# Performance work log

Measured on AMD Instinct MI355X. Metric: run time of the kernel, lower is better.

## Reference

```python
import jax, jax.numpy as jnp
import numpy as np

HOP = 2
N = 16384
HIDDEN = 64


def setup_inputs() -> dict:
    key = jax.random.key(0)
    k1, k2, k3 = jax.random.split(key, 3)
    user_embs = jax.random.normal(k1, (N, HIDDEN), dtype=jnp.float32)
    adj = jax.random.uniform(k2, (N, N), dtype=jnp.float32)
    # xavier-uniform-like scale for [2*HIDDEN, HIDDEN] weights
    limit = float(np.sqrt(6.0 / (2 * HIDDEN + HIDDEN)))
    W = jax.random.uniform(k3, (HOP, 2 * HIDDEN, HIDDEN), dtype=jnp.float32,
                           minval=-limit, maxval=limit)
    return {"user_embs": user_embs, "adj": adj, "W": W}


def reference(user_embs, adj, W):
    # DiffNet social GCN: hop rounds of aggregate -> concat -> dense -> tanh.
    # Dropout omitted (eval mode, training=False).
    x = user_embs
    for k in range(HOP):
        agg = adj @ x                                  # [N, H] neighbor aggregation
        x = jnp.tanh(jnp.concatenate([agg, x], axis=1) @ W[k])  # [N, H]
    return x
```

## Files before the change

kernel.cpp:

```cpp
#include <hip/hip_runtime.h>
#include <hip/hip_bf16.h>
#include <math.h>

#define NROWS 16384
#define HID 64
#define KSPLIT 8
#define KCH (NROWS / KSPLIT)

typedef __attribute__((ext_vector_type(8))) __bf16 bf16x8;
typedef __attribute__((ext_vector_type(4))) float f32x4;

__device__ inline f32x4 mfma16(bf16x8 a, bf16x8 b, f32x4 c) {
    return __builtin_amdgcn_mfma_f32_16x16x32_bf16(a, b, c, 0, 0, 0);
}

__device__ inline void split8v(const f32x4 v0, const f32x4 v1, bf16x8& h, bf16x8& l) {
    float f[8] = {v0[0], v0[1], v0[2], v0[3], v1[0], v1[1], v1[2], v1[3]};
#pragma unroll
    for (int j = 0; j < 8; ++j) {
        __bf16 hh = (__bf16)f[j];
        h[j] = hh;
        l[j] = (__bf16)(f[j] - (float)hh);
    }
}

__global__ __launch_bounds__(256) void pack_b(const float* __restrict__ x,
                                              __bf16* __restrict__ hi,
                                              __bf16* __restrict__ lo) {
    __shared__ float tile[32 * 64];
    const int kb = blockIdx.x;
    const f32x4* src = (const f32x4*)(x + (size_t)kb * 32 * 64);
    f32x4* dst = (f32x4*)tile;
    dst[threadIdx.x] = src[threadIdx.x];
    dst[threadIdx.x + 256] = src[threadIdx.x + 256];
    __syncthreads();
    const int t = threadIdx.x >> 6;
    const int l = threadIdx.x & 63;
    const int col = (t << 4) + (l & 15);
    const int krow = (l >> 4) * 8;
    bf16x8 h8, l8;
#pragma unroll
    for (int j = 0; j < 8; ++j) {
        float v = tile[(krow + j) * 64 + col];
        __bf16 hh = (__bf16)v;
        h8[j] = hh;
        l8[j] = (__bf16)(v - (float)hh);
    }
    const size_t base = (((size_t)kb * 4 + t) * 64 + l) * 8;
    *(bf16x8*)(hi + base) = h8;
    *(bf16x8*)(lo + base) = l8;
}

__global__ __launch_bounds__(256, 1) void gemm_partial(const float* __restrict__ adj,
                                                       const __bf16* __restrict__ Bhi,
                                                       const __bf16* __restrict__ Blo,
                                                       float* __restrict__ partial) {
    const int lane = threadIdx.x & 63;
    const int wv = threadIdx.x >> 6;
    const int rt = blockIdx.x & 31;
    const int ks = blockIdx.x >> 5;
    const int rbase = rt * 512 + wv * 128;
    const int rq = lane & 15;
    const int kq = lane >> 4;

    f32x4 acc[8][4];
#pragma unroll
    for (int g = 0; g < 8; ++g)
#pragma unroll
        for (int t = 0; t < 4; ++t) acc[g][t] = f32x4{0.f, 0.f, 0.f, 0.f};

    const float* ap = adj + (size_t)(rbase + rq) * NROWS + ks * KCH + kq * 8;
    const int kk0 = ks * KCH;

    for (int kk = 0; kk < KCH; kk += 32) {
        f32x4 av0[4][2];
#pragma unroll
        for (int g = 0; g < 4; ++g) {
            const f32x4* a = (const f32x4*)(ap + (size_t)(g * 16) * NROWS + kk);
            av0[g][0] = a[0];
            av0[g][1] = a[1];
        }
        const size_t bb = ((size_t)((kk0 + kk) >> 5) * 4) * 512 + (size_t)lane * 8;
        bf16x8 bh[4], bl[4];
#pragma unroll
        for (int t = 0; t < 4; ++t) {
            bh[t] = *(const bf16x8*)(Bhi + bb + (size_t)t * 512);
            bl[t] = *(const bf16x8*)(Blo + bb + (size_t)t * 512);
        }
        f32x4 av1[4][2];
#pragma unroll
        for (int g = 0; g < 4; ++g) {
            const f32x4* a = (const f32x4*)(ap + (size_t)((g + 4) * 16) * NROWS + kk);
            av1[g][0] = a[0];
            av1[g][1] = a[1];
        }
#pragma unroll
        for (int g = 0; g < 4; ++g) {
            bf16x8 ah, al;
            split8v(av0[g][0], av0[g][1], ah, al);
#pragma unroll
            for (int t = 0; t < 4; ++t) {
                acc[g][t] = mfma16(ah, bh[t], acc[g][t]);
                acc[g][t] = mfma16(ah, bl[t], acc[g][t]);
                acc[g][t] = mfma16(al, bh[t], acc[g][t]);
            }
        }
#pragma unroll
        for (int g = 0; g < 4; ++g) {
            bf16x8 ah, al;
            split8v(av1[g][0], av1[g][1], ah, al);
#pragma unroll
            for (int t = 0; t < 4; ++t) {
                acc[g + 4][t] = mfma16(ah, bh[t], acc[g + 4][t]);
                acc[g + 4][t] = mfma16(ah, bl[t], acc[g + 4][t]);
                acc[g + 4][t] = mfma16(al, bh[t], acc[g + 4][t]);
            }
        }
    }

    float* pp = partial + (size_t)ks * (NROWS * HID) + (size_t)rbase * HID;
#pragma unroll
    for (int g = 0; g < 8; ++g)
#pragma unroll
        for (int t = 0; t < 4; ++t)
#pragma unroll
            for (int r = 0; r < 4; ++r)
                __builtin_nontemporal_store(acc[g][t][r],
                    pp + (g * 16 + kq * 4 + r) * HID + t * 16 + rq);
}

__global__ __launch_bounds__(256) void reduce_dense(const float* __restrict__ partial,
                                                    const float* __restrict__ xin,
                                                    const float* __restrict__ W,
                                                    float* __restrict__ xout,
                                                    __bf16* __restrict__ hi,
                                                    __bf16* __restrict__ lo) {
    __shared__ float wsm[128 * 64];
    __shared__ float xt[32][64];
    const f32x4* wsrc = (const f32x4*)W;
    f32x4* wdst = (f32x4*)wsm;
#pragma unroll
    for (int i = 0; i < 8; ++i) wdst[threadIdx.x + 256 * i] = wsrc[threadIdx.x + 256 * i];
    __syncthreads();

    const int lane = threadIdx.x & 63;
    const int wv = threadIdx.x >> 6;
    const int r0 = blockIdx.x * 32 + wv * 8;
#pragma unroll 2
    for (int i = 0; i < 8; ++i) {
        const int r = r0 + i;
        float av = 0.f;
#pragma unroll
        for (int ks = 0; ks < KSPLIT; ++ks)
            av += partial[(size_t)ks * (NROWS * HID) + (size_t)r * HID + lane];
        const float xv = xin[(size_t)r * HID + lane];
        float z = 0.f;
#pragma unroll
        for (int j = 0; j < 64; ++j) z += __shfl(av, j) * wsm[j * 64 + lane];
#pragma unroll
        for (int j = 0; j < 64; ++j) z += __shfl(xv, j) * wsm[(64 + j) * 64 + lane];
        const float v = tanhf(z);
        xout[(size_t)r * HID + lane] = v;
        xt[wv * 8 + i][lane] = v;
    }

    if (hi != nullptr) {
        __syncthreads();
        const int t = threadIdx.x >> 6;
        const int l = threadIdx.x & 63;
        const int col = (t << 4) + (l & 15);
        const int krow = (l >> 4) * 8;
        bf16x8 h8, l8;
#pragma unroll
        for (int j = 0; j < 8; ++j) {
            float v = xt[krow + j][col];
            __bf16 hh = (__bf16)v;
            h8[j] = hh;
            l8[j] = (__bf16)(v - (float)hh);
        }
        const size_t base = (((size_t)blockIdx.x * 4 + t) * 64 + l) * 8;
        *(bf16x8*)(hi + base) = h8;
        *(bf16x8*)(lo + base) = l8;
    }
}

extern "C" void kernel_launch(void* const* d_in, const int* in_sizes, int n_in,
                              void* d_out, int out_size, void* d_ws, size_t ws_size,
                              hipStream_t stream) {
    const float* x0 = (const float*)d_in[0];
    const float* adj = (const float*)d_in[1];
    const float* W = (const float*)d_in[2];
    float* out = (float*)d_out;

    char* ws = (char*)d_ws;
    __bf16* Bhi = (__bf16*)(ws);
    __bf16* Blo = (__bf16*)(ws + (2u << 20));
    float* partial = (float*)(ws + (4u << 20));
    float* x1 = (float*)(ws + (36u << 20));

    pack_b<<<512, 256, 0, stream>>>(x0, Bhi, Blo);
    gemm_partial<<<KSPLIT * 32, 256, 0, stream>>>(adj, Bhi, Blo, partial);
    reduce_dense<<<512, 256, 0, stream>>>(partial, x0, W, x1, Bhi, Blo);
    gemm_partial<<<KSPLIT * 32, 256, 0, stream>>>(adj, Bhi, Blo, partial);
    reduce_dense<<<512, 256, 0, stream>>>(partial, x1, W + 128 * 64, out, nullptr, nullptr);
}
```

Before: 453.8 us.

## Double per-wave row tile to 256 rows and pipeline adj loads across quarters

Each wave now covers 256 rows (16 row groups) instead of 128, so every B fragment loaded from the packed hi/lo buffers feeds twice as many MFMAs. The adj loads are split into four quarters, each issued before the previous quarter is consumed, to overlap global loads with the MFMA work. KSPLIT goes from 8 to 16 to keep 256 blocks, which doubles the partial-sum buffer and the traffic in the reduce step. The accumulator grows to 256 floats per lane, which raises register pressure and risks spills.

Measured after the change: 486.5 us. 1.07x slower.

```diff
diff --git a/kernel.cpp b/kernel.cpp
--- a/kernel.cpp
+++ b/kernel.cpp
@@ -4,7 +4,7 @@
 
 #define NROWS 16384
 #define HID 64
-#define KSPLIT 8
+#define KSPLIT 16
 #define KCH (NROWS / KSPLIT)
 
 typedef __attribute__((ext_vector_type(8))) __bf16 bf16x8;
@@ -57,29 +57,46 @@
                                                        float* __restrict__ partial) {
     const int lane = threadIdx.x & 63;
     const int wv = threadIdx.x >> 6;
-    const int rt = blockIdx.x & 31;
-    const int ks = blockIdx.x >> 5;
-    const int rbase = rt * 512 + wv * 128;
+    const int rt = blockIdx.x & 15;
+    const int ks = blockIdx.x >> 4;
+    const int rbase = rt * 1024 + wv * 256;
     const int rq = lane & 15;
     const int kq = lane >> 4;
 
-    f32x4 acc[8][4];
-#pragma unroll
-    for (int g = 0; g < 8; ++g)
+    f32x4 acc[16][4];
+#pragma unroll
+    for (int g = 0; g < 16; ++g)
 #pragma unroll
         for (int t = 0; t < 4; ++t) acc[g][t] = f32x4{0.f, 0.f, 0.f, 0.f};
 
     const float* ap = adj + (size_t)(rbase + rq) * NROWS + ks * KCH + kq * 8;
     const int kk0 = ks * KCH;
 
+#define LOADQ(q, gbase, kk)                                                     \
+    {                                                                           \
+        _Pragma("unroll") for (int g = 0; g < 4; ++g) {                         \
+            const f32x4* a =                                                    \
+                (const f32x4*)(ap + (size_t)(((gbase) + g) * 16) * NROWS + kk); \
+            q[g][0] = a[0];                                                     \
+            q[g][1] = a[1];                                                     \
+        }                                                                       \
+    }
+#define CONSQ(q, gbase)                                                         \
+    {                                                                           \
+        _Pragma("unroll") for (int g = 0; g < 4; ++g) {                         \
+            bf16x8 ah, al;                                                      \
+            split8v(q[g][0], q[g][1], ah, al);                                  \
+            _Pragma("unroll") for (int t = 0; t < 4; ++t) {                     \
+                acc[(gbase) + g][t] = mfma16(ah, bh[t], acc[(gbase) + g][t]);   \
+                acc[(gbase) + g][t] = mfma16(ah, bl[t], acc[(gbase) + g][t]);   \
+                acc[(gbase) + g][t] = mfma16(al, bh[t], acc[(gbase) + g][t]);   \
+            }                                                                   \
+        }                                                                       \
+    }
+
     for (int kk = 0; kk < KCH; kk += 32) {
-        f32x4 av0[4][2];
-#pragma unroll
-        for (int g = 0; g < 4; ++g) {
-            const f32x4* a = (const f32x4*)(ap + (size_t)(g * 16) * NROWS + kk);
-            av0[g][0] = a[0];
-            av0[g][1] = a[1];
-        }
+        f32x4 q0[4][2], q1[4][2], q2[4][2], q3[4][2];
+        LOADQ(q0, 0, kk);
         const size_t bb = ((size_t)((kk0 + kk) >> 5) * 4) * 512 + (size_t)lane * 8;
         bf16x8 bh[4], bl[4];
 #pragma unroll
@@ -87,40 +104,18 @@
             bh[t] = *(const bf16x8*)(Bhi + bb + (size_t)t * 512);
             bl[t] = *(const bf16x8*)(Blo + bb + (size_t)t * 512);
         }
-        f32x4 av1[4][2];
-#pragma unroll
-        for (int g = 0; g < 4; ++g) {
-            const f32x4* a = (const f32x4*)(ap + (size_t)((g + 4) * 16) * NROWS + kk);
-            av1[g][0] = a[0];
-            av1[g][1] = a[1];
-        }
-#pragma unroll
-        for (int g = 0; g < 4; ++g) {
-            bf16x8 ah, al;
-            split8v(av0[g][0], av0[g][1], ah, al);
-#pragma unroll
-            for (int t = 0; t < 4; ++t) {
-                acc[g][t] = mfma16(ah, bh[t], acc[g][t]);
-                acc[g][t] = mfma16(ah, bl[t], acc[g][t]);
-                acc[g][t] = mfma16(al, bh[t], acc[g][t]);
-            }
-        }
-#pragma unroll
-        for (int g = 0; g < 4; ++g) {
-            bf16x8 ah, al;
-            split8v(av1[g][0], av1[g][1], ah, al);
-#pragma unroll
-            for (int t = 0; t < 4; ++t) {
-                acc[g + 4][t] = mfma16(ah, bh[t], acc[g + 4][t]);
-                acc[g + 4][t] = mfma16(ah, bl[t], acc[g + 4][t]);
-                acc[g + 4][t] = mfma16(al, bh[t], acc[g + 4][t]);
-            }
-        }
+        LOADQ(q1, 4, kk);
+        CONSQ(q0, 0);
+        LOADQ(q2, 8, kk);
+        CONSQ(q1, 4);
+        LOADQ(q3, 12, kk);
+        CONSQ(q2, 8);
+        CONSQ(q3, 12);
     }
 
     float* pp = partial + (size_t)ks * (NROWS * HID) + (size_t)rbase * HID;
 #pragma unroll
-    for (int g = 0; g < 8; ++g)
+    for (int g = 0; g < 16; ++g)
 #pragma unroll
         for (int t = 0; t < 4; ++t)
 #pragma unroll
@@ -196,11 +191,11 @@
     __bf16* Bhi = (__bf16*)(ws);
     __bf16* Blo = (__bf16*)(ws + (2u << 20));
     float* partial = (float*)(ws + (4u << 20));
-    float* x1 = (float*)(ws + (36u << 20));
+    float* x1 = (float*)(ws + (68u << 20));
 
     pack_b<<<512, 256, 0, stream>>>(x0, Bhi, Blo);
-    gemm_partial<<<KSPLIT * 32, 256, 0, stream>>>(adj, Bhi, Blo, partial);
+    gemm_partial<<<KSPLIT * 16, 256, 0, stream>>>(adj, Bhi, Blo, partial);
     reduce_dense<<<512, 256, 0, stream>>>(partial, x0, W, x1, Bhi, Blo);
-    gemm_partial<<<KSPLIT * 32, 256, 0, stream>>>(adj, Bhi, Blo, partial);
+    gemm_partial<<<KSPLIT * 16, 256, 0, stream>>>(adj, Bhi, Blo, partial);
     reduce_dense<<<512, 256, 0, stream>>>(partial, x1, W + 128 * 64, out, nullptr, nullptr);
 }
```
